# Performance work log

Measured on AMD Instinct MI355X. Metric: run time of the kernel, lower is better.

The kernel has to match this reference:

```python
import jax, jax.numpy as jnp
import numpy as np

B, H, S, D = 4, 16, 2048, 64

def setup_inputs() -> dict:
    key = jax.random.key(0)
    kq, kk, kv = jax.random.split(key, 3)
    Q = jax.random.normal(kq, (B, H, S, D), dtype=jnp.float32)
    K = jax.random.normal(kk, (B, H, S, D), dtype=jnp.float32)
    V = jax.random.normal(kv, (B, H, S, D), dtype=jnp.float32)
    return {"Q": Q, "K": K, "V": V}

def reference(Q, K, V):
    d_model = Q.shape[-1]
    # [B,H,S,S] scores matrix, materialized as in the original (unfused SDPA)
    scores = jnp.einsum('bhqd,bhkd->bhqk', Q, K) / jnp.sqrt(jnp.float32(d_model))
    attention = jax.nn.softmax(scores, axis=-1)
    out = jnp.einsum('bhqk,bhkd->bhqd', attention, V)
    return out
```

## Files before the change

### kernel.cpp

```cpp
#include <hip/hip_runtime.h>
#include <hip/hip_bf16.h>

namespace {

constexpr int kSeq = 2048;
constexpr int kD   = 64;
constexpr int kBH  = 64;
constexpr int kQB  = 128;
constexpr int kBN  = 64;
constexpr int kNT  = kSeq / kBN;
constexpr int kPs  = 72;

typedef __attribute__((ext_vector_type(8))) short bf16x8;
typedef __attribute__((ext_vector_type(4))) float f32x4;
typedef __attribute__((ext_vector_type(2))) unsigned int u32x2;

__device__ __forceinline__ unsigned short f2bf(float f) {
  unsigned int u = __builtin_bit_cast(unsigned int, f);
  u += 0x7fffu + ((u >> 16) & 1u);
  return (unsigned short)(u >> 16);
}

__device__ __forceinline__ unsigned int pkbf(float a, float b) {
#if __has_builtin(__builtin_amdgcn_cvt_pk_bf16_f32)
  typedef __attribute__((ext_vector_type(2))) __bf16 bfv2;
  bfv2 r = __builtin_amdgcn_cvt_pk_bf16_f32(a, b);
  return __builtin_bit_cast(unsigned int, r);
#else
  unsigned int ua = __builtin_bit_cast(unsigned int, a) + 0x8000u;
  unsigned int ub = __builtin_bit_cast(unsigned int, b) + 0x8000u;
  return __builtin_amdgcn_perm(ub, ua, 0x07060302);
#endif
}

__device__ __forceinline__ float fexp2(float x) {
#if __has_builtin(__builtin_amdgcn_exp2f)
  return __builtin_amdgcn_exp2f(x);
#else
  return exp2f(x);
#endif
}

__device__ __forceinline__ void load16(const unsigned short* g, unsigned short* l) {
  __builtin_amdgcn_global_load_lds(
      (const __attribute__((address_space(1))) unsigned int*)g,
      (__attribute__((address_space(3))) unsigned int*)l, 16, 0, 0);
}

__global__ __launch_bounds__(256) void prep(
    const float* __restrict__ K, const float* __restrict__ V,
    unsigned short* __restrict__ Kbf, unsigned short* __restrict__ Vt) {
  __shared__ float sTf[kD * 65];
  const int tid = threadIdx.x;
  const int bh = blockIdx.x >> 5;
  const int t0 = (blockIdx.x & 31) * 64;
  const float* Kb = K + ((size_t)bh * kSeq + t0) * kD;
  const float* Vb = V + ((size_t)bh * kSeq + t0) * kD;
  unsigned short* Ko = Kbf + ((size_t)bh * kSeq + t0) * kD;
#pragma unroll
  for (int t = 0; t < 4; ++t) {
    const int idx = tid + t * 256;
    const int row = idx >> 4;
    const int c4  = (idx & 15) * 4;
    const float4 k4 = *(const float4*)(Kb + row * kD + c4);
    u32x2 kp = {pkbf(k4.x, k4.y), pkbf(k4.z, k4.w)};
    *(u32x2*)(Ko + row * kD + c4) = kp;
    const float4 v4 = *(const float4*)(Vb + row * kD + c4);
    sTf[(c4 + 0) * 65 + row] = v4.x;
    sTf[(c4 + 1) * 65 + row] = v4.y;
    sTf[(c4 + 2) * 65 + row] = v4.z;
    sTf[(c4 + 3) * 65 + row] = v4.w;
  }
  __syncthreads();
  const int d = tid >> 2, q = tid & 3;
  const float* ts = &sTf[d * 65 + q * 16];
  float p[16];
#pragma unroll
  for (int j = 0; j < 16; ++j) p[j] = ts[j];
  uint4 a, b;
  a.x = pkbf(p[0], p[1]);   a.y = pkbf(p[2], p[3]);
  a.z = pkbf(p[4], p[5]);   a.w = pkbf(p[6], p[7]);
  b.x = pkbf(p[8], p[9]);   b.y = pkbf(p[10], p[11]);
  b.z = pkbf(p[12], p[13]); b.w = pkbf(p[14], p[15]);
  unsigned short* vo = Vt + ((size_t)bh * kD + d) * kSeq + t0 + q * 16;
  *(uint4*)(vo)     = a;
  *(uint4*)(vo + 8) = b;
}

__global__ __launch_bounds__(512, 6) void fattn5(
    const float* __restrict__ Q, const unsigned short* __restrict__ Kbf,
    const unsigned short* __restrict__ Vt, float* __restrict__ O) {
  __shared__ unsigned short sK[2][kBN * kD];
  __shared__ unsigned short sV[2][kD * kBN];
  __shared__ unsigned short sP[8 * 16 * kD];

  const int tid  = threadIdx.x;
  const int wave = tid >> 6;
  const int lane = tid & 63;
  const int quad = lane >> 4;
  const int l16  = lane & 15;
  const int swz  = l16 & 7;

  const int x  = blockIdx.x & 7;
  const int j  = blockIdx.x >> 3;
  const int bh = x * 8 + (j >> 4);
  const int q0 = (j & 15) * kQB;
  const size_t kb = (size_t)bh * kSeq * kD;

  constexpr float cs = 0.18033688011112042f;

  bf16x8 qf[2];
  {
    const float* qr = Q + kb + (size_t)(q0 + wave * 16 + l16) * kD + quad * 8;
#pragma unroll
    for (int kc = 0; kc < 2; ++kc)
#pragma unroll
      for (int jj = 0; jj < 8; ++jj)
        qf[kc][jj] = (short)f2bf(qr[kc * 32 + jj] * cs);
  }

  bf16x8 ones;
#pragma unroll
  for (int jj = 0; jj < 8; ++jj) ones[jj] = (short)0x3F80;

  const int r0 = tid >> 3, c0 = (tid & 7) ^ (r0 & 7);
  const unsigned short* kg0 = Kbf + kb + r0 * kD + c0 * 8;
  const unsigned short* vg0 = Vt + kb + r0 * kSeq + c0 * 8;

  f32x4 o[4];
#pragma unroll
  for (int dt = 0; dt < 4; ++dt) o[dt] = (f32x4){0.f, 0.f, 0.f, 0.f};
  f32x4 lacc = (f32x4){0.f, 0.f, 0.f, 0.f};

  unsigned short* pw = &sP[(wave * 16 + l16) * kD];

  load16(kg0, &sK[0][wave * 512]);
  load16(vg0, &sV[0][wave * 512]);

  for (int t = 0; t < kNT; ++t) {
    const int p = t & 1;
    __syncthreads();
    if (t + 1 < kNT) {
      const int pn = p ^ 1;
      load16(kg0 + (size_t)(t + 1) * kBN * kD, &sK[pn][wave * 512]);
      load16(vg0 + (t + 1) * kBN, &sV[pn][wave * 512]);
    }
    const unsigned short* sKp = sK[p];
    const unsigned short* sVp = sV[p];

    f32x4 s[4];
#pragma unroll
    for (int nt = 0; nt < 4; ++nt) s[nt] = (f32x4){0.f, 0.f, 0.f, 0.f};
#pragma unroll
    for (int kc = 0; kc < 2; ++kc)
#pragma unroll
      for (int nt = 0; nt < 4; ++nt) {
        const bf16x8 kf = *(const bf16x8*)&sKp[(nt * 16 + l16) * kD +
                                              (((kc * 4 + quad) ^ swz) * 8)];
        s[nt] = __builtin_amdgcn_mfma_f32_16x16x32_bf16(kf, qf[kc], s[nt], 0, 0, 0);
      }

#pragma unroll
    for (int nt = 0; nt < 4; ++nt) {
      const float p0 = fexp2(s[nt][0]);
      const float p1 = fexp2(s[nt][1]);
      const float p2 = fexp2(s[nt][2]);
      const float p3 = fexp2(s[nt][3]);
      u32x2 pp = {pkbf(p0, p1), pkbf(p2, p3)};
      const int pc = ((nt * 2 + (quad >> 1)) ^ swz) * 8 + (quad & 1) * 4;
      *(u32x2*)&pw[pc] = pp;
    }

#pragma unroll
    for (int kc = 0; kc < 2; ++kc) {
      const bf16x8 af = *(const bf16x8*)&pw[((kc * 4 + quad) ^ swz) * 8];
#pragma unroll
      for (int dt = 0; dt < 4; ++dt) {
        const bf16x8 vf = *(const bf16x8*)&sVp[(dt * 16 + l16) * kBN +
                                               (((kc * 4 + quad) ^ swz) * 8)];
        o[dt] = __builtin_amdgcn_mfma_f32_16x16x32_bf16(af, vf, o[dt], 0, 0, 0);
      }
      lacc = __builtin_amdgcn_mfma_f32_16x16x32_bf16(af, ones, lacc, 0, 0, 0);
    }
  }

  float* Ob = O + kb + (size_t)(q0 + wave * 16) * kD;
#pragma unroll
  for (int r = 0; r < 4; ++r) {
    const float inv = 1.f / lacc[r];
#pragma unroll
    for (int dt = 0; dt < 4; ++dt)
      Ob[(quad * 4 + r) * kD + dt * 16 + l16] = o[dt][r] * inv;
  }
}

__global__ __launch_bounds__(256, 4) void fattn_fb(
    const float* __restrict__ Q, const float* __restrict__ K,
    const float* __restrict__ V, float* __restrict__ O) {
  __shared__ unsigned short sK[kBN * kPs];
  __shared__ unsigned short sV[kD * kPs];
  __shared__ unsigned short sP[4 * 16 * kPs];
  const int tid = threadIdx.x, wave = tid >> 6, lane = tid & 63;
  const int quad = lane >> 4, l16 = lane & 15;
  const int bh = blockIdx.x >> 5, q0 = (blockIdx.x & 31) * 64;
  const float* Qb = Q + (size_t)bh * kSeq * kD;
  const float* Kb = K + (size_t)bh * kSeq * kD;
  const float* Vb = V + (size_t)bh * kSeq * kD;
  bf16x8 qf[2];
  {
    const float* qr = Qb + (size_t)(q0 + wave * 16 + l16) * kD + quad * 8;
#pragma unroll
    for (int kc = 0; kc < 2; ++kc)
#pragma unroll
      for (int jj = 0; jj < 8; ++jj) qf[kc][jj] = (short)f2bf(qr[kc * 32 + jj]);
  }
  f32x4 o[4];
#pragma unroll
  for (int dt = 0; dt < 4; ++dt) o[dt] = (f32x4){0.f, 0.f, 0.f, 0.f};
  float lsum[4] = {0.f, 0.f, 0.f, 0.f};
  constexpr float cs = 0.18033688011112042f;
  unsigned short* pw = &sP[wave * 16 * kPs];
  for (int kv0 = 0; kv0 < kSeq; kv0 += kBN) {
    __syncthreads();
#pragma unroll
    for (int t = 0; t < 4; ++t) {
      const int idx = tid + t * 256;
      const int row = idx >> 4, c4 = (idx & 15) * 4;
      const float4 k4 = *(const float4*)(Kb + (size_t)(kv0 + row) * kD + c4);
      unsigned short* kd = &sK[row * kPs + c4];
      kd[0] = f2bf(k4.x); kd[1] = f2bf(k4.y); kd[2] = f2bf(k4.z); kd[3] = f2bf(k4.w);
      const float4 v4 = *(const float4*)(Vb + (size_t)(kv0 + row) * kD + c4);
      sV[(c4 + 0) * kPs + row] = f2bf(v4.x);
      sV[(c4 + 1) * kPs + row] = f2bf(v4.y);
      sV[(c4 + 2) * kPs + row] = f2bf(v4.z);
      sV[(c4 + 3) * kPs + row] = f2bf(v4.w);
    }
    __syncthreads();
    f32x4 s[4];
#pragma unroll
    for (int nt = 0; nt < 4; ++nt) s[nt] = (f32x4){0.f, 0.f, 0.f, 0.f};
#pragma unroll
    for (int kc = 0; kc < 2; ++kc)
#pragma unroll
      for (int nt = 0; nt < 4; ++nt) {
        const bf16x8 kf = *(const bf16x8*)&sK[(nt * 16 + l16) * kPs + kc * 32 + quad * 8];
        s[nt] = __builtin_amdgcn_mfma_f32_16x16x32_bf16(qf[kc], kf, s[nt], 0, 0, 0);
      }
#pragma unroll
    for (int nt = 0; nt < 4; ++nt)
#pragma unroll
      for (int r = 0; r < 4; ++r) {
        const float p = fexp2(s[nt][r] * cs);
        lsum[r] += p;
        pw[(quad * 4 + r) * kPs + nt * 16 + l16] = f2bf(p);
      }
#pragma unroll
    for (int kc = 0; kc < 2; ++kc) {
      const bf16x8 af = *(const bf16x8*)&pw[l16 * kPs + kc * 32 + quad * 8];
#pragma unroll
      for (int dt = 0; dt < 4; ++dt) {
        const bf16x8 vf = *(const bf16x8*)&sV[(dt * 16 + l16) * kPs + kc * 32 + quad * 8];
        o[dt] = __builtin_amdgcn_mfma_f32_16x16x32_bf16(af, vf, o[dt], 0, 0, 0);
      }
    }
  }
#pragma unroll
  for (int r = 0; r < 4; ++r)
#pragma unroll
    for (int off = 1; off < 16; off <<= 1)
      lsum[r] += __shfl_xor(lsum[r], off, 64);
  float* Ob = O + (size_t)bh * kSeq * kD + (size_t)(q0 + wave * 16) * kD;
#pragma unroll
  for (int r = 0; r < 4; ++r) {
    const float inv = 1.f / lsum[r];
#pragma unroll
    for (int dt = 0; dt < 4; ++dt)
      Ob[(quad * 4 + r) * kD + dt * 16 + l16] = o[dt][r] * inv;
  }
}

}

extern "C" void kernel_launch(void* const* d_in, const int* in_sizes, int n_in,
                              void* d_out, int out_size, void* d_ws, size_t ws_size,
                              hipStream_t stream) {
  const float* Q = (const float*)d_in[0];
  const float* K = (const float*)d_in[1];
  const float* V = (const float*)d_in[2];
  float* Oo = (float*)d_out;
  const size_t need = (size_t)2 * kBH * kSeq * kD * sizeof(unsigned short);
  if (ws_size >= need) {
    unsigned short* Kbf = (unsigned short*)d_ws;
    unsigned short* Vt  = Kbf + (size_t)kBH * kSeq * kD;
    prep<<<dim3(kBH * (kSeq / 64)), dim3(256), 0, stream>>>(K, V, Kbf, Vt);
    fattn5<<<dim3(kBH * (kSeq / kQB)), dim3(512), 0, stream>>>(Q, Kbf, Vt, Oo);
  } else {
    fattn_fb<<<dim3(kBH * (kSeq / 64)), dim3(256), 0, stream>>>(Q, K, V, Oo);
  }
}
```

Baseline: 213.8 us.

## Give each wave two 16-row query tiles, halving waves per block

The block now has 4 waves instead of 8, and each wave computes two 16-row query tiles. Every K and V fragment read from shared memory is reused across two MFMAs, which halves LDS traffic per unit of compute. Each thread now issues two K and two V global-to-LDS loads per tile. The costs are more registers per thread (two sets of accumulators and scores), fewer waves per block to hide latency, and a lower launch-bounds occupancy target.

New measurement: 211.7 us. About the same (-1.0%).

```diff
diff --git a/kernel.cpp b/kernel.cpp
--- a/kernel.cpp
+++ b/kernel.cpp
@@ -87,12 +87,12 @@
   *(uint4*)(vo + 8) = b;
 }
 
-__global__ __launch_bounds__(512, 6) void fattn5(
+__global__ __launch_bounds__(256, 3) void fattn6(
     const float* __restrict__ Q, const unsigned short* __restrict__ Kbf,
     const unsigned short* __restrict__ Vt, float* __restrict__ O) {
   __shared__ unsigned short sK[2][kBN * kD];
   __shared__ unsigned short sV[2][kD * kBN];
-  __shared__ unsigned short sP[8 * 16 * kD];
+  __shared__ unsigned short sP[4 * 32 * kD];
 
   const int tid  = threadIdx.x;
   const int wave = tid >> 6;
@@ -109,88 +109,113 @@
 
   constexpr float cs = 0.18033688011112042f;
 
-  bf16x8 qf[2];
-  {
-    const float* qr = Q + kb + (size_t)(q0 + wave * 16 + l16) * kD + quad * 8;
+  bf16x8 qf[2][2];
+#pragma unroll
+  for (int mt = 0; mt < 2; ++mt) {
+    const float* qr =
+        Q + kb + (size_t)(q0 + wave * 32 + mt * 16 + l16) * kD + quad * 8;
 #pragma unroll
     for (int kc = 0; kc < 2; ++kc)
 #pragma unroll
       for (int jj = 0; jj < 8; ++jj)
-        qf[kc][jj] = (short)f2bf(qr[kc * 32 + jj] * cs);
+        qf[mt][kc][jj] = (short)f2bf(qr[kc * 32 + jj] * cs);
   }
 
   bf16x8 ones;
 #pragma unroll
   for (int jj = 0; jj < 8; ++jj) ones[jj] = (short)0x3F80;
 
-  const int r0 = tid >> 3, c0 = (tid & 7) ^ (r0 & 7);
+  const int i0 = tid, i1 = tid + 256;
+  const int r0 = i0 >> 3, c0 = (i0 & 7) ^ (r0 & 7);
+  const int r1 = i1 >> 3, c1 = (i1 & 7) ^ (r1 & 7);
   const unsigned short* kg0 = Kbf + kb + r0 * kD + c0 * 8;
+  const unsigned short* kg1 = Kbf + kb + r1 * kD + c1 * 8;
   const unsigned short* vg0 = Vt + kb + r0 * kSeq + c0 * 8;
-
-  f32x4 o[4];
-#pragma unroll
-  for (int dt = 0; dt < 4; ++dt) o[dt] = (f32x4){0.f, 0.f, 0.f, 0.f};
-  f32x4 lacc = (f32x4){0.f, 0.f, 0.f, 0.f};
-
-  unsigned short* pw = &sP[(wave * 16 + l16) * kD];
-
-  load16(kg0, &sK[0][wave * 512]);
-  load16(vg0, &sV[0][wave * 512]);
+  const unsigned short* vg1 = Vt + kb + r1 * kSeq + c1 * 8;
+
+  f32x4 o[2][4];
+#pragma unroll
+  for (int mt = 0; mt < 2; ++mt)
+#pragma unroll
+    for (int dt = 0; dt < 4; ++dt) o[mt][dt] = (f32x4){0.f, 0.f, 0.f, 0.f};
+  f32x4 lacc[2] = {(f32x4){0.f, 0.f, 0.f, 0.f}, (f32x4){0.f, 0.f, 0.f, 0.f}};
+
+  unsigned short* pwA = &sP[(wave * 32 + l16) * kD];
+  unsigned short* pwB = pwA + 16 * kD;
+
+  load16(kg0, &sK[0][i0 * 8]);
+  load16(kg1, &sK[0][i1 * 8]);
+  load16(vg0, &sV[0][i0 * 8]);
+  load16(vg1, &sV[0][i1 * 8]);
 
   for (int t = 0; t < kNT; ++t) {
     const int p = t & 1;
     __syncthreads();
     if (t + 1 < kNT) {
       const int pn = p ^ 1;
-      load16(kg0 + (size_t)(t + 1) * kBN * kD, &sK[pn][wave * 512]);
-      load16(vg0 + (t + 1) * kBN, &sV[pn][wave * 512]);
+      const size_t ko = (size_t)(t + 1) * kBN * kD;
+      const int vo = (t + 1) * kBN;
+      load16(kg0 + ko, &sK[pn][i0 * 8]);
+      load16(kg1 + ko, &sK[pn][i1 * 8]);
+      load16(vg0 + vo, &sV[pn][i0 * 8]);
+      load16(vg1 + vo, &sV[pn][i1 * 8]);
     }
     const unsigned short* sKp = sK[p];
     const unsigned short* sVp = sV[p];
 
-    f32x4 s[4];
-#pragma unroll
-    for (int nt = 0; nt < 4; ++nt) s[nt] = (f32x4){0.f, 0.f, 0.f, 0.f};
+    f32x4 sA[4], sB[4];
+#pragma unroll
+    for (int nt = 0; nt < 4; ++nt) {
+      sA[nt] = (f32x4){0.f, 0.f, 0.f, 0.f};
+      sB[nt] = (f32x4){0.f, 0.f, 0.f, 0.f};
+    }
 #pragma unroll
     for (int kc = 0; kc < 2; ++kc)
 #pragma unroll
       for (int nt = 0; nt < 4; ++nt) {
         const bf16x8 kf = *(const bf16x8*)&sKp[(nt * 16 + l16) * kD +
                                               (((kc * 4 + quad) ^ swz) * 8)];
-        s[nt] = __builtin_amdgcn_mfma_f32_16x16x32_bf16(kf, qf[kc], s[nt], 0, 0, 0);
+        sA[nt] = __builtin_amdgcn_mfma_f32_16x16x32_bf16(kf, qf[0][kc], sA[nt], 0, 0, 0);
+        sB[nt] = __builtin_amdgcn_mfma_f32_16x16x32_bf16(kf, qf[1][kc], sB[nt], 0, 0, 0);
       }
 
 #pragma unroll
     for (int nt = 0; nt < 4; ++nt) {
-      const float p0 = fexp2(s[nt][0]);
-      const float p1 = fexp2(s[nt][1]);
-      const float p2 = fexp2(s[nt][2]);
-      const float p3 = fexp2(s[nt][3]);
-      u32x2 pp = {pkbf(p0, p1), pkbf(p2, p3)};
       const int pc = ((nt * 2 + (quad >> 1)) ^ swz) * 8 + (quad & 1) * 4;
-      *(u32x2*)&pw[pc] = pp;
+      u32x2 ppA = {pkbf(fexp2(sA[nt][0]), fexp2(sA[nt][1])),
+                   pkbf(fexp2(sA[nt][2]), fexp2(sA[nt][3]))};
+      *(u32x2*)&pwA[pc] = ppA;
+      u32x2 ppB = {pkbf(fexp2(sB[nt][0]), fexp2(sB[nt][1])),
+                   pkbf(fexp2(sB[nt][2]), fexp2(sB[nt][3]))};
+      *(u32x2*)&pwB[pc] = ppB;
     }
 
 #pragma unroll
     for (int kc = 0; kc < 2; ++kc) {
-      const bf16x8 af = *(const bf16x8*)&pw[((kc * 4 + quad) ^ swz) * 8];
+      const int ac = ((kc * 4 + quad) ^ swz) * 8;
+      const bf16x8 afA = *(const bf16x8*)&pwA[ac];
+      const bf16x8 afB = *(const bf16x8*)&pwB[ac];
+      lacc[0] = __builtin_amdgcn_mfma_f32_16x16x32_bf16(afA, ones, lacc[0], 0, 0, 0);
+      lacc[1] = __builtin_amdgcn_mfma_f32_16x16x32_bf16(afB, ones, lacc[1], 0, 0, 0);
 #pragma unroll
       for (int dt = 0; dt < 4; ++dt) {
-        const bf16x8 vf = *(const bf16x8*)&sVp[(dt * 16 + l16) * kBN +
-                                               (((kc * 4 + quad) ^ swz) * 8)];
-        o[dt] = __builtin_amdgcn_mfma_f32_16x16x32_bf16(af, vf, o[dt], 0, 0, 0);
-      }
-      lacc = __builtin_amdgcn_mfma_f32_16x16x32_bf16(af, ones, lacc, 0, 0, 0);
-    }
-  }
-
-  float* Ob = O + kb + (size_t)(q0 + wave * 16) * kD;
-#pragma unroll
-  for (int r = 0; r < 4; ++r) {
-    const float inv = 1.f / lacc[r];
-#pragma unroll
-    for (int dt = 0; dt < 4; ++dt)
-      Ob[(quad * 4 + r) * kD + dt * 16 + l16] = o[dt][r] * inv;
+        const bf16x8 vf = *(const bf16x8*)&sVp[(dt * 16 + l16) * kBN + ac];
+        o[0][dt] = __builtin_amdgcn_mfma_f32_16x16x32_bf16(afA, vf, o[0][dt], 0, 0, 0);
+        o[1][dt] = __builtin_amdgcn_mfma_f32_16x16x32_bf16(afB, vf, o[1][dt], 0, 0, 0);
+      }
+    }
+  }
+
+#pragma unroll
+  for (int mt = 0; mt < 2; ++mt) {
+    float* Ob = O + kb + (size_t)(q0 + wave * 32 + mt * 16) * kD;
+#pragma unroll
+    for (int r = 0; r < 4; ++r) {
+      const float inv = 1.f / lacc[mt][r];
+#pragma unroll
+      for (int dt = 0; dt < 4; ++dt)
+        Ob[(quad * 4 + r) * kD + dt * 16 + l16] = o[mt][dt][r] * inv;
+    }
   }
 }
 
@@ -293,7 +318,7 @@
     unsigned short* Kbf = (unsigned short*)d_ws;
     unsigned short* Vt  = Kbf + (size_t)kBH * kSeq * kD;
     prep<<<dim3(kBH * (kSeq / 64)), dim3(256), 0, stream>>>(K, V, Kbf, Vt);
-    fattn5<<<dim3(kBH * (kSeq / kQB)), dim3(512), 0, stream>>>(Q, Kbf, Vt, Oo);
+    fattn6<<<dim3(kBH * (kSeq / kQB)), dim3(256), 0, stream>>>(Q, Kbf, Vt, Oo);
   } else {
     fattn_fb<<<dim3(kBH * (kSeq / 64)), dim3(256), 0, stream>>>(Q, K, V, Oo);
   }
```
